# Optimization experiments

Measured on AMD Instinct MI355X. Metric: run time of the kernel, lower is better.

Reference implementation:

```python
import jax, jax.numpy as jnp
import numpy as np

N_ROWS = 8192
EMBED_DIM = 256


def setup_inputs() -> dict:
    key = jax.random.key(0)
    k1, k2, k3, k4, k5 = jax.random.split(key, 5)
    M = jax.random.normal(k1, (N_ROWS, EMBED_DIM), dtype=jnp.float32)
    N = jax.random.normal(k2, (N_ROWS, EMBED_DIM), dtype=jnp.float32)
    # gate_w: nn.Linear(embed_dim, 1) -> weight [1, d], bias [1]; gate_b extra scalar param [1]
    Wg = jax.random.normal(k3, (1, EMBED_DIM), dtype=jnp.float32) * 0.06
    bg = jax.random.normal(k4, (1,), dtype=jnp.float32) * 0.1
    gate_b = jax.random.normal(k5, (1,), dtype=jnp.float32) * 0.1
    return {"M": M, "N": N, "Wg": Wg, "bg": bg, "gate_b": gate_b, "iseval": 0}


def reference(M, N, Wg, bg, gate_b, iseval):
    # mt: [n, n] cross-similarity scores
    mt = jnp.matmul(N, M.T)
    if not iseval:
        # training branch: zero out the diagonal (mt - diag(diag(mt)))
        n = mt.shape[0]
        idx = jnp.arange(n)
        mt = mt.at[idx, idx].set(0.0)
    else:
        # eval branch: zero out the first row
        mt = mt.at[0].set(0.0)
    attn_weight = jax.nn.softmax(mt, axis=-1)          # [n, n]
    out_attn = jnp.matmul(attn_weight, M)              # [n, d]
    gate = jax.nn.sigmoid(jnp.matmul(out_attn, Wg.T) + bg + gate_b)  # [n, 1]
    boosted = out_attn * gate + N * (1.0 - gate)       # [n, d]
    return boosted[:, None, None, :]                   # [n, 1, 1, d]
```

## Files before the change

### kernel.cpp

```cpp
#include <hip/hip_runtime.h>


constexpr int EMBED = 256;
constexpr int BQ = 64;
constexpr int BJ = 32;
constexpr int NT = 256;

constexpr int MH_OFF = 0;
constexpr int MH_BUF = 16384;
constexpr int P_OFF  = 32768;
constexpr int A_OFF  = 37888;
constexpr int LDS_SZ = 38144;

typedef _Float16 half8 __attribute__((ext_vector_type(8)));
typedef _Float16 half4v __attribute__((ext_vector_type(4)));
typedef float f32x4 __attribute__((ext_vector_type(4)));
typedef short short8v __attribute__((ext_vector_type(8)));

static __device__ __forceinline__ f32x4 mfma16(half8 a, half8 b, f32x4 c) {
    return __builtin_amdgcn_mfma_f32_16x16x32_f16(a, b, c, 0, 0, 0);
}
static __device__ __forceinline__ short f2h(float x) {
    return (short)__builtin_bit_cast(unsigned short, (_Float16)x);
}

__global__ void prep(const float* __restrict__ M,
                     short* __restrict__ MhG, short* __restrict__ MtG) {
    __shared__ float L[16 * 260];
    const int r0 = blockIdx.x * 16;
    const int t = threadIdx.x;
    const int pj = t >> 4, pc = (t & 15) * 16;
    {
        const float* src = M + (size_t)(r0 + pj) * EMBED + pc;
        float4 v[4];
        #pragma unroll
        for (int i = 0; i < 4; ++i) v[i] = ((const float4*)src)[i];
        short* hd = MhG + (size_t)(r0 + pj) * EMBED + pc;
        #pragma unroll
        for (int i = 0; i < 2; ++i) {
            float4 a = v[2 * i], b = v[2 * i + 1];
            short8v h;
            h[0]=f2h(a.x); h[1]=f2h(a.y); h[2]=f2h(a.z); h[3]=f2h(a.w);
            h[4]=f2h(b.x); h[5]=f2h(b.y); h[6]=f2h(b.z); h[7]=f2h(b.w);
            *(short8v*)(hd + 8 * i) = h;
        }
        #pragma unroll
        for (int i = 0; i < 4; ++i)
            *(float4*)(L + pj * 260 + pc + 4 * i) = v[i];
    }
    __syncthreads();
    {
        const int d = t;
        const int tile = r0 >> 5, jh = (r0 >> 4) & 1;
        short* dst = MtG + (size_t)tile * (BJ * EMBED) + d * BJ + jh * 16;
        #pragma unroll
        for (int g2 = 0; g2 < 2; ++g2) {
            short8v w;
            #pragma unroll
            for (int e = 0; e < 8; ++e) w[e] = f2h(L[(g2 * 8 + e) * 260 + d]);
            *(short8v*)(dst + g2 * 8) = w;
        }
    }
}

__launch_bounds__(NT, 2)
__global__ void attn(const short* __restrict__ MhG, const short* __restrict__ MtG,
                     const float* __restrict__ Ng, const int* __restrict__ iseval_p,
                     float* __restrict__ O0out, short* __restrict__ Ofp,
                     float* __restrict__ MLm, float* __restrict__ MLl, int n)
{
    __shared__ __align__(16) char smem[LDS_SZ];

    const int t = threadIdx.x, lane = t & 63, wave = t >> 6;
    const int quad = lane >> 4, mn = lane & 15;
    const int bid = blockIdx.x;
    const int s  = (bid & 7) >> 1;
    const int qb = ((bid >> 3) << 1) | (bid & 1);
    const int q0 = qb * BQ;
    const int jbase = s * (n >> 2);
    const int jb32 = jbase / BJ;
    const int ntiles = (n >> 2) / BJ;
    const int iseval = *iseval_p;
    const int qg = wave;
    const int dq = wave;
    const int qrow = q0 + qg * 16 + mn;
    const int swz = (mn & 7) << 4;

    const int sj = t >> 3;
    const int sc7 = t & 7;

    const float L2E = 1.4426950408889634f;
    half8 Qf[8];
    {
        const float* np = Ng + (size_t)qrow * EMBED;
        #pragma unroll
        for (int kk = 0; kk < 8; ++kk) {
            const float* pp = np + kk * 32 + quad * 8;
            float4 a = *(const float4*)pp, b = *(const float4*)(pp + 4);
            half8 h;
            h[0]=(_Float16)(a.x*L2E); h[1]=(_Float16)(a.y*L2E);
            h[2]=(_Float16)(a.z*L2E); h[3]=(_Float16)(a.w*L2E);
            h[4]=(_Float16)(b.x*L2E); h[5]=(_Float16)(b.y*L2E);
            h[6]=(_Float16)(b.z*L2E); h[7]=(_Float16)(b.w*L2E);
            Qf[kk] = h;
        }
    }

    f32x4 O[4][4];
    #pragma unroll
    for (int qi = 0; qi < 4; ++qi)
        #pragma unroll
        for (int dt = 0; dt < 4; ++dt) O[qi][dt] = (f32x4){0.f, 0.f, 0.f, 0.f};

    float m_reg = -1e30f, l_reg = 0.f;

    {
        const short* src = MhG + (size_t)(jbase + sj) * EMBED + sc7 * 32;
        #pragma unroll
        for (int i = 0; i < 4; ++i) {
            short8v v = ((const short8v*)src)[i];
            int off = (sj * 512 + sc7 * 64 + i * 16) ^ ((sj & 7) << 4);
            *(short8v*)(smem + MH_OFF + off) = v;
        }
    }

    half8 Mtf[4];
    short8v stv[4];

    for (int tt = 0; tt < ntiles; ++tt) {
        const int p = tt & 1;
        __syncthreads();

        if (tt + 1 < ntiles) {
            const short* src = MhG + (size_t)(jbase + (tt + 1) * BJ + sj) * EMBED + sc7 * 32;
            #pragma unroll
            for (int i = 0; i < 4; ++i) stv[i] = ((const short8v*)src)[i];
        }
        {
            const short* mtb = MtG + (size_t)(jb32 + tt) * (BJ * EMBED);
            #pragma unroll
            for (int dt = 0; dt < 4; ++dt)
                Mtf[dt] = *(const half8*)(mtb + (dq * 64 + dt * 16 + mn) * BJ + quad * 8);
        }

        f32x4 s0 = (f32x4){0,0,0,0}, s1 = (f32x4){0,0,0,0};
        {
            const int base = MH_OFF + p * MH_BUF;
            #pragma unroll
            for (int kk = 0; kk < 8; ++kk) {
                int o0 = (mn * 512 + kk * 64 + quad * 16) ^ swz;
                half8 k0 = *(const half8*)(smem + base + o0);
                half8 k1 = *(const half8*)(smem + base + 8192 + o0);
                s0 = mfma16(k0, Qf[kk], s0);
                s1 = mfma16(k1, Qf[kk], s1);
            }
        }

        {
            float sv[8] = {s0[0], s0[1], s0[2], s0[3], s1[0], s1[1], s1[2], s1[3]};
            if (iseval) {
                if (qrow == 0) {
                    #pragma unroll
                    for (int i = 0; i < 8; ++i) sv[i] = 0.f;
                }
            } else {
                int dj = qrow - (jbase + tt * BJ);
                #pragma unroll
                for (int i = 0; i < 4; ++i) {
                    if (dj == quad * 4 + i)      sv[i]     = 0.f;
                    if (dj == 16 + quad * 4 + i) sv[4 + i] = 0.f;
                }
            }
            float mx = sv[0];
            #pragma unroll
            for (int i = 1; i < 8; ++i) mx = fmaxf(mx, sv[i]);
            mx = fmaxf(mx, __shfl_xor(mx, 16));
            mx = fmaxf(mx, __shfl_xor(mx, 32));
            float m_new = fmaxf(m_reg, mx);
            float alpha = exp2f(m_reg - m_new);
            float pv8[8], ps = 0.f;
            #pragma unroll
            for (int i = 0; i < 8; ++i) { pv8[i] = exp2f(sv[i] - m_new); ps += pv8[i]; }
            ps += __shfl_xor(ps, 16);
            ps += __shfl_xor(ps, 32);
            m_reg = m_new;
            l_reg = l_reg * alpha + ps;
            half4v h0, h1;
            #pragma unroll
            for (int i = 0; i < 4; ++i) { h0[i] = (_Float16)pv8[i]; h1[i] = (_Float16)pv8[4 + i]; }
            char* pb = smem + P_OFF + (qg * 16 + mn) * 80;
            *(half4v*)(pb + quad * 8)      = h0;
            *(half4v*)(pb + 32 + quad * 8) = h1;
            if (quad == 0)
                ((float*)(smem + A_OFF))[qg * 16 + mn] = alpha;
        }
        __syncthreads();

        #pragma unroll
        for (int qi = 0; qi < 4; ++qi) {
            half8 pf = *(const half8*)(smem + P_OFF + (qi * 16 + mn) * 80 + quad * 16);
            f32x4 al = *(const f32x4*)(smem + A_OFF + (qi * 16 + quad * 4) * 4);
            #pragma unroll
            for (int dt = 0; dt < 4; ++dt) {
                f32x4 o = O[qi][dt];
                o[0] *= al[0]; o[1] *= al[1]; o[2] *= al[2]; o[3] *= al[3];
                O[qi][dt] = mfma16(pf, Mtf[dt], o);
            }
        }

        if (tt + 1 < ntiles) {
            #pragma unroll
            for (int i = 0; i < 4; ++i) {
                int off = (sj * 512 + sc7 * 64 + i * 16) ^ ((sj & 7) << 4);
                *(short8v*)(smem + MH_OFF + (p ^ 1) * MH_BUF + off) = stv[i];
            }
        }
    }

    if (s == 0) {
        #pragma unroll
        for (int qi = 0; qi < 4; ++qi)
            #pragma unroll
            for (int dt = 0; dt < 4; ++dt) {
                int col = dq * 64 + dt * 16 + mn;
                #pragma unroll
                for (int r = 0; r < 4; ++r)
                    O0out[(size_t)(q0 + qi * 16 + quad * 4 + r) * EMBED + col] = O[qi][dt][r];
            }
    } else {
        short* dst = Ofp + (size_t)(s - 1) * n * EMBED;
        #pragma unroll
        for (int qi = 0; qi < 4; ++qi)
            #pragma unroll
            for (int dt = 0; dt < 4; ++dt) {
                int col = dq * 64 + dt * 16 + mn;
                #pragma unroll
                for (int r = 0; r < 4; ++r)
                    dst[(size_t)(q0 + qi * 16 + quad * 4 + r) * EMBED + col] = f2h(O[qi][dt][r]);
            }
    }
    if (lane < 16) {
        MLm[s * n + q0 + qg * 16 + mn] = m_reg;
        MLl[s * n + q0 + qg * 16 + mn] = l_reg;
    }
}

__global__ void combine4(const float* __restrict__ O0, const short* __restrict__ Ofp,
                         const float* __restrict__ MLm, const float* __restrict__ MLl,
                         const float* __restrict__ Ng, const float* __restrict__ Wg,
                         const float* __restrict__ bg, const float* __restrict__ gb,
                         float* __restrict__ out, int n)
{
    const int t = threadIdx.x;
    const int row = blockIdx.x * 16 + (t >> 4);
    const int c = t & 15;
    float ms[4], ls[4];
    #pragma unroll
    for (int k = 0; k < 4; ++k) { ms[k] = MLm[k * n + row]; ls[k] = MLl[k * n + row]; }
    float m = fmaxf(fmaxf(ms[0], ms[1]), fmaxf(ms[2], ms[3]));
    float w[4], lsum = 0.f;
    #pragma unroll
    for (int k = 0; k < 4; ++k) { w[k] = exp2f(ms[k] - m); lsum += w[k] * ls[k]; }
    float linv = 1.f / lsum;

    float acc[16];
    {
        const float4* o0 = (const float4*)(O0 + (size_t)row * EMBED + c * 16);
        #pragma unroll
        for (int i = 0; i < 4; ++i) {
            float4 v = o0[i];
            acc[4*i+0] = w[0] * v.x; acc[4*i+1] = w[0] * v.y;
            acc[4*i+2] = w[0] * v.z; acc[4*i+3] = w[0] * v.w;
        }
    }
    #pragma unroll
    for (int k = 1; k < 4; ++k) {
        const short* op = Ofp + (size_t)(k - 1) * n * EMBED + (size_t)row * EMBED + c * 16;
        half8 a = *(const half8*)op, b = *(const half8*)(op + 8);
        #pragma unroll
        for (int i = 0; i < 8; ++i) {
            acc[i]     += w[k] * (float)a[i];
            acc[8 + i] += w[k] * (float)b[i];
        }
    }
    float dot = 0.f;
    #pragma unroll
    for (int i = 0; i < 16; ++i) { acc[i] *= linv; dot += acc[i] * Wg[c * 16 + i]; }
    dot += __shfl_xor(dot, 1);
    dot += __shfl_xor(dot, 2);
    dot += __shfl_xor(dot, 4);
    dot += __shfl_xor(dot, 8);
    float g = 1.f / (1.f + __expf(-(dot + bg[0] + gb[0])));
    const float4* n4 = (const float4*)(Ng + (size_t)row * EMBED + c * 16);
    float4* o4 = (float4*)(out + (size_t)row * EMBED + c * 16);
    #pragma unroll
    for (int i = 0; i < 4; ++i) {
        float4 nn = n4[i];
        float4 res;
        res.x = acc[4*i+0] * g + nn.x * (1.f - g);
        res.y = acc[4*i+1] * g + nn.y * (1.f - g);
        res.z = acc[4*i+2] * g + nn.z * (1.f - g);
        res.w = acc[4*i+3] * g + nn.w * (1.f - g);
        o4[i] = res;
    }
}

extern "C" void kernel_launch(void* const* d_in, const int* in_sizes, int n_in,
                              void* d_out, int out_size, void* d_ws, size_t ws_size,
                              hipStream_t stream) {
    const float* M      = (const float*)d_in[0];
    const float* N      = (const float*)d_in[1];
    const float* Wgp    = (const float*)d_in[2];
    const float* bgp    = (const float*)d_in[3];
    const float* gbp    = (const float*)d_in[4];
    const int*   iseval = (const int*)d_in[5];
    float* out = (float*)d_out;

    int n = in_sizes[0] / EMBED;
    short* MhG = (short*)d_ws;
    short* MtG = MhG + (size_t)n * EMBED;
    short* Ofp = MtG + (size_t)n * EMBED;
    float* MLm = (float*)(Ofp + (size_t)3 * n * EMBED);
    float* MLl = MLm + 4 * n;

    hipLaunchKernelGGL(prep, dim3(n / 16), dim3(NT), 0, stream, M, MhG, MtG);
    hipLaunchKernelGGL(attn, dim3((n / BQ) * 4), dim3(NT), 0, stream,
                       MhG, MtG, N, iseval, out, Ofp, MLm, MLl, n);
    hipLaunchKernelGGL(combine4, dim3(n / 16), dim3(NT), 0, stream,
                       out, Ofp, MLm, MLl, N, Wgp, bgp, gbp, out, n);
}
```

Baseline: 211.0 us.

## Load K tiles directly into registers and double-buffer P/alpha LDS

```diff
diff --git a/kernel.cpp b/kernel.cpp
--- a/kernel.cpp
+++ b/kernel.cpp
@@ -6,11 +6,11 @@
 constexpr int BJ = 32;
 constexpr int NT = 256;
 
-constexpr int MH_OFF = 0;
-constexpr int MH_BUF = 16384;
-constexpr int P_OFF  = 32768;
-constexpr int A_OFF  = 37888;
-constexpr int LDS_SZ = 38144;
+constexpr int P_OFF  = 0;
+constexpr int P_BUF  = 5120;
+constexpr int A_OFF  = 10240;
+constexpr int A_BUF  = 256;
+constexpr int LDS_SZ = 10752;
 
 typedef _Float16 half8 __attribute__((ext_vector_type(8)));
 typedef _Float16 half4v __attribute__((ext_vector_type(4)));
@@ -84,10 +84,6 @@
     const int qg = wave;
     const int dq = wave;
     const int qrow = q0 + qg * 16 + mn;
-    const int swz = (mn & 7) << 4;
-
-    const int sj = t >> 3;
-    const int sc7 = t & 7;
 
     const float L2E = 1.4426950408889634f;
     half8 Qf[8];
@@ -114,45 +110,37 @@
 
     float m_reg = -1e30f, l_reg = 0.f;
 
-    {
-        const short* src = MhG + (size_t)(jbase + sj) * EMBED + sc7 * 32;
-        #pragma unroll
-        for (int i = 0; i < 4; ++i) {
-            short8v v = ((const short8v*)src)[i];
-            int off = (sj * 512 + sc7 * 64 + i * 16) ^ ((sj & 7) << 4);
-            *(short8v*)(smem + MH_OFF + off) = v;
-        }
-    }
-
-    half8 Mtf[4];
-    short8v stv[4];
+    const short* kb0 = MhG + (size_t)(jbase + mn) * EMBED + quad * 8;
+
+    half8 K0[8], K1[8], Mtf[4];
+    #pragma unroll
+    for (int kk = 0; kk < 8; ++kk) {
+        K0[kk] = *(const half8*)(kb0 + kk * 32);
+        K1[kk] = *(const half8*)(kb0 + 16 * EMBED + kk * 32);
+    }
+    {
+        const short* mtb = MtG + (size_t)jb32 * (BJ * EMBED);
+        #pragma unroll
+        for (int dt = 0; dt < 4; ++dt)
+            Mtf[dt] = *(const half8*)(mtb + (dq * 64 + dt * 16 + mn) * BJ + quad * 8);
+    }
 
     for (int tt = 0; tt < ntiles; ++tt) {
         const int p = tt & 1;
-        __syncthreads();
+
+        f32x4 s0 = (f32x4){0,0,0,0}, s1 = (f32x4){0,0,0,0};
+        #pragma unroll
+        for (int kk = 0; kk < 8; ++kk) {
+            s0 = mfma16(K0[kk], Qf[kk], s0);
+            s1 = mfma16(K1[kk], Qf[kk], s1);
+        }
 
         if (tt + 1 < ntiles) {
-            const short* src = MhG + (size_t)(jbase + (tt + 1) * BJ + sj) * EMBED + sc7 * 32;
-            #pragma unroll
-            for (int i = 0; i < 4; ++i) stv[i] = ((const short8v*)src)[i];
-        }
-        {
-            const short* mtb = MtG + (size_t)(jb32 + tt) * (BJ * EMBED);
-            #pragma unroll
-            for (int dt = 0; dt < 4; ++dt)
-                Mtf[dt] = *(const half8*)(mtb + (dq * 64 + dt * 16 + mn) * BJ + quad * 8);
-        }
-
-        f32x4 s0 = (f32x4){0,0,0,0}, s1 = (f32x4){0,0,0,0};
-        {
-            const int base = MH_OFF + p * MH_BUF;
+            const short* kb = kb0 + (size_t)(tt + 1) * (BJ * EMBED);
             #pragma unroll
             for (int kk = 0; kk < 8; ++kk) {
-                int o0 = (mn * 512 + kk * 64 + quad * 16) ^ swz;
-                half8 k0 = *(const half8*)(smem + base + o0);
-                half8 k1 = *(const half8*)(smem + base + 8192 + o0);
-                s0 = mfma16(k0, Qf[kk], s0);
-                s1 = mfma16(k1, Qf[kk], s1);
+                K0[kk] = *(const half8*)(kb + kk * 32);
+                K1[kk] = *(const half8*)(kb + 16 * EMBED + kk * 32);
             }
         }
 
@@ -188,18 +176,19 @@
             half4v h0, h1;
             #pragma unroll
             for (int i = 0; i < 4; ++i) { h0[i] = (_Float16)pv8[i]; h1[i] = (_Float16)pv8[4 + i]; }
-            char* pb = smem + P_OFF + (qg * 16 + mn) * 80;
+            char* pb = smem + P_OFF + p * P_BUF + (qg * 16 + mn) * 80;
             *(half4v*)(pb + quad * 8)      = h0;
             *(half4v*)(pb + 32 + quad * 8) = h1;
             if (quad == 0)
-                ((float*)(smem + A_OFF))[qg * 16 + mn] = alpha;
-        }
+                ((float*)(smem + A_OFF + p * A_BUF))[qg * 16 + mn] = alpha;
+        }
+
         __syncthreads();
 
         #pragma unroll
         for (int qi = 0; qi < 4; ++qi) {
-            half8 pf = *(const half8*)(smem + P_OFF + (qi * 16 + mn) * 80 + quad * 16);
-            f32x4 al = *(const f32x4*)(smem + A_OFF + (qi * 16 + quad * 4) * 4);
+            half8 pf = *(const half8*)(smem + P_OFF + p * P_BUF + (qi * 16 + mn) * 80 + quad * 16);
+            f32x4 al = *(const f32x4*)(smem + A_OFF + p * A_BUF + (qi * 16 + quad * 4) * 4);
             #pragma unroll
             for (int dt = 0; dt < 4; ++dt) {
                 f32x4 o = O[qi][dt];
@@ -209,11 +198,10 @@
         }
 
         if (tt + 1 < ntiles) {
-            #pragma unroll
-            for (int i = 0; i < 4; ++i) {
-                int off = (sj * 512 + sc7 * 64 + i * 16) ^ ((sj & 7) << 4);
-                *(short8v*)(smem + MH_OFF + (p ^ 1) * MH_BUF + off) = stv[i];
-            }
+            const short* mtb = MtG + (size_t)(jb32 + tt + 1) * (BJ * EMBED);
+            #pragma unroll
+            for (int dt = 0; dt < 4; ++dt)
+                Mtf[dt] = *(const half8*)(mtb + (dq * 64 + dt * 16 + mn) * BJ + quad * 8);
         }
     }
 
```

Result: slower. 348.5 us (+65.2%).
